# Optimization experiments

Hardware: AMD Instinct MI355X
Metric: run time of the kernel (lower is better)

## Reference

```python
import jax, jax.numpy as jnp
import numpy as np

FACTOR = 5      # ProbAttention sampling factor
NHEAD = 8
LN_EPS = 1e-5


def pos_encoding(L, d):
    pos = np.arange(L, dtype=np.float32)[:, None]
    div = np.exp(np.arange(0, d, 2, dtype=np.float32) * (-np.log(10000.0) / d))
    pe = np.zeros((L, d), np.float32)
    pe[:, 0::2] = np.sin(pos * div)
    pe[:, 1::2] = np.cos(pos * div)
    return jnp.asarray(pe)


def layer_norm(x, s, b):
    mu = x.mean(-1, keepdims=True)
    var = ((x - mu) ** 2).mean(-1, keepdims=True)
    return (x - mu) * jax.lax.rsqrt(var + LN_EPS) * s + b


def prob_attention(x4, key):
    # x4: [B, L, H, D]; self-attention (Q=K=V=x4), mask_flag=False
    B, L, H, D = x4.shape
    q = jnp.transpose(x4, (0, 2, 1, 3))  # [B,H,L,D]
    u = max(1, min(FACTOR * int(np.ceil(np.log(L))), L))  # L_Q == L_K
    # random K-sampling: per-query random subset of keys (shared across B,H)
    idx = jax.random.randint(key, (L, u), 0, L)
    k_s = q[:, :, idx, :]                                # [B,H,L,u,D] irregular gather
    qk_s = jnp.einsum('bhld,bhlsd->bhls', q, k_s)        # [B,H,L,u]
    M = qk_s.max(-1) - qk_s.sum(-1) / L                  # sparsity measure
    _, top = jax.lax.top_k(M, u)                         # [B,H,u] active queries
    q_red = jnp.take_along_axis(q, top[..., None], axis=2)   # [B,H,u,D]
    scale = 1.0 / jnp.sqrt(jnp.float32(D))
    scores = jnp.einsum('bhud,bhkd->bhuk', q_red, q) * scale  # reduced-query scores
    attn = jax.nn.softmax(scores, axis=-1)
    ctx_top = jnp.einsum('bhuk,bhkd->bhud', attn, q)     # V == q here
    # initial context = mean of V (mask_flag=False), scatter top-query results
    ctx = jnp.broadcast_to(q.mean(axis=2, keepdims=True), (B, H, L, D))
    bi = jnp.arange(B)[:, None, None]
    hi = jnp.arange(H)[None, :, None]
    ctx = ctx.at[bi, hi, top].set(ctx_top)
    return jnp.transpose(ctx, (0, 2, 1, 3))  # [B,L,H,D]


def encoder_layer(x4, ln1_s, ln1_b, w1, b1, w2, b2, ln2_s, ln2_b, key):
    B, L, H, D = x4.shape
    new = prob_attention(x4, key)
    x = x4.reshape(B, L, H * D)
    x = layer_norm(x + new.reshape(B, L, H * D), ln1_s, ln1_b)
    # conv1/conv2 with kernel_size=1 == pointwise linears
    y = jax.nn.gelu(jnp.einsum('bld,fd->blf', x, w1) + b1, approximate=False)
    y = jnp.einsum('blf,df->bld', y, w2) + b2
    x = layer_norm(x + y, ln2_s, ln2_b)
    return x.reshape(B, L, H, D)


def distil(x4, factor=2):
    # DistilledAttention: mean-pool over `factor` timesteps (zero-pad to multiple)
    B, L, H, D = x4.shape
    pad = (-L) % factor
    if pad:
        x4 = jnp.pad(x4, ((0, 0), (0, pad), (0, 0), (0, 0)))
    return x4.reshape(B, -1, factor, H, D).mean(axis=2)


def setup_inputs() -> dict:
    key = jax.random.key(0)
    B, L, IN, D, DF, NL = 8, 4096, 64, 512, 2048, 3
    ks = jax.random.split(key, 16)
    s = 0.02
    return {
        'x': jax.random.normal(ks[0], (B, L, IN), jnp.float32),
        'emb_w': jax.random.normal(ks[1], (D, IN), jnp.float32) * s,
        'emb_b': jnp.zeros((D,), jnp.float32),
        'ln1_s': jnp.ones((NL, D), jnp.float32),
        'ln1_b': jnp.zeros((NL, D), jnp.float32),
        'w1': jax.random.normal(ks[2], (NL, DF, D), jnp.float32) * s,
        'b1': jnp.zeros((NL, DF), jnp.float32),
        'w2': jax.random.normal(ks[3], (NL, D, DF), jnp.float32) * s,
        'b2': jnp.zeros((NL, D), jnp.float32),
        'ln2_s': jnp.ones((NL, D), jnp.float32),
        'ln2_b': jnp.zeros((NL, D), jnp.float32),
        'out_w': jax.random.normal(ks[4], (D, D), jnp.float32) * s,
        'out_b': jnp.zeros((D,), jnp.float32),
    }


def reference(x, emb_w, emb_b, ln1_s, ln1_b, w1, b1, w2, b2, ln2_s, ln2_b, out_w, out_b):
    B, L, _ = x.shape
    D = emb_w.shape[0]
    hd = D // NHEAD
    h = jnp.einsum('bli,di->bld', x, emb_w) + emb_b
    h = h + pos_encoding(L, D)[None]
    h = h.reshape(B, L, NHEAD, hd)
    NL = ln1_s.shape[0]
    rkey = jax.random.key(42)  # deterministic ProbSparse sampling
    for i in range(NL):
        h = encoder_layer(h, ln1_s[i], ln1_b[i], w1[i], b1[i], w2[i], b2[i],
                          ln2_s[i], ln2_b[i], jax.random.fold_in(rkey, i))
        if i < NL - 1:
            h = distil(h)
    B2, L2 = h.shape[:2]
    h = h.reshape(B2, L2, D)
    return jnp.einsum('bld,od->blo', h, out_w) + out_b
```

## Files before the change

kernel.cpp:

```cpp
#include <hip/hip_runtime.h>
#include <hip/hip_bf16.h>
#include <math.h>


typedef short short8 __attribute__((ext_vector_type(8)));
typedef float f32x4 __attribute__((ext_vector_type(4)));
typedef unsigned int uint;

__host__ __device__ inline void tf2x32(unsigned k0, unsigned k1,
                                       unsigned x0, unsigned x1,
                                       unsigned& o0, unsigned& o1) {
  unsigned ks2 = k0 ^ k1 ^ 0x1BD11BDAu;
#define TF_R(x, r) x0 += x1; x1 = ((x1 << (r)) | (x1 >> (32 - (r)))); x1 ^= x0;
  x0 += k0; x1 += k1;
  TF_R(x1,13) TF_R(x1,15) TF_R(x1,26) TF_R(x1,6)
  x0 += k1; x1 += ks2 + 1u;
  TF_R(x1,17) TF_R(x1,29) TF_R(x1,16) TF_R(x1,24)
  x0 += ks2; x1 += k0 + 2u;
  TF_R(x1,13) TF_R(x1,15) TF_R(x1,26) TF_R(x1,6)
  x0 += k0; x1 += k1 + 3u;
  TF_R(x1,17) TF_R(x1,29) TF_R(x1,16) TF_R(x1,24)
  x0 += k1; x1 += ks2 + 4u;
  TF_R(x1,13) TF_R(x1,15) TF_R(x1,26) TF_R(x1,6)
  x0 += ks2; x1 += k0 + 5u;
#undef TF_R
  o0 = x0; o1 = x1;
}

__global__ void k_idx(int* __restrict__ idx, unsigned k2a, unsigned k2b,
                      int n, int mask) {
  int j = blockIdx.x * 256 + threadIdx.x;
  if (j >= n) return;
  unsigned o0, o1;
  tf2x32(k2a, k2b, 0u, (unsigned)j, o0, o1);
  idx[j] = (int)((o0 ^ o1) & (unsigned)mask);
}

__global__ void k_pe(float* __restrict__ pe) {
  int t = blockIdx.x * 256 + threadIdx.x;
  int l = t >> 9, d = t & 511;
  double div = exp((double)(d & ~1) * (-9.210340371976184 / 512.0));
  double ang = (double)l * div;
  pe[t] = (float)((d & 1) ? cos(ang) : sin(ang));
}

__global__ __launch_bounds__(256) void k_embed(const float* __restrict__ x,
    const float* __restrict__ W, const float* __restrict__ eb,
    const float* __restrict__ pe, float* __restrict__ out) {
  __shared__ __align__(16) float xs[16][64];
  int r0 = blockIdx.x * 16;
  int t = threadIdx.x;
  ((float4*)&xs[0][0])[t] = ((const float4*)(x + (size_t)r0 * 64))[t];
  __syncthreads();
  int d0 = t, d1 = t + 256;
  float acc0[16], acc1[16];
#pragma unroll
  for (int r = 0; r < 16; r++) { acc0[r] = 0.f; acc1[r] = 0.f; }
  for (int k = 0; k < 64; k++) {
    float w0 = W[d0 * 64 + k], w1 = W[d1 * 64 + k];
#pragma unroll
    for (int r = 0; r < 16; r++) {
      float xv = xs[r][k];
      acc0[r] = fmaf(xv, w0, acc0[r]);
      acc1[r] = fmaf(xv, w1, acc1[r]);
    }
  }
  float eb0 = eb[d0], eb1 = eb[d1];
#pragma unroll
  for (int r = 0; r < 16; r++) {
    int row = r0 + r;
    int l = row & 4095;
    out[(size_t)row * 512 + d0] = acc0[r] + eb0 + pe[(size_t)l * 512 + d0];
    out[(size_t)row * 512 + d1] = acc1[r] + eb1 + pe[(size_t)l * 512 + d1];
  }
}

__global__ __launch_bounds__(256) void k_colmean1(const float* __restrict__ X,
    double* __restrict__ part, int L, int S) {
  int seg = blockIdx.x, bh = blockIdx.y, b = bh >> 3, h = bh & 7;
  int w = threadIdx.x >> 6, d = threadIdx.x & 63;
  int rows = L / S, r0 = seg * rows;
  const float* base = X + (size_t)b * L * 512 + h * 64 + d;
  double s = 0.0;
  for (int l = r0 + w; l < r0 + rows; l += 4) s += (double)base[(size_t)l * 512];
  __shared__ double red[4][64];
  red[w][d] = s;
  __syncthreads();
  if (w == 0)
    part[((size_t)bh * S + seg) * 64 + d] =
        red[0][d] + red[1][d] + red[2][d] + red[3][d];
}

__global__ void k_colmean2(const double* __restrict__ part,
    float* __restrict__ meanq, int L, int S) {
  int bh = blockIdx.x, d = threadIdx.x;
  const double* p = part + (size_t)bh * S * 64 + d;
  double s = 0.0;
  for (int seg = 0; seg < S; seg++) s += p[seg * 64];
  meanq[bh * 64 + d] = (float)(s / (double)L);
}

__global__ __launch_bounds__(256) void k_M(const float* __restrict__ X,
    const int* __restrict__ idx, float* __restrict__ Mout, int L, int Lsh,
    int u, float invL) {
  int w = threadIdx.x >> 6, lane = threadIdx.x & 63;
  int gl = blockIdx.x * 4 + w;
  int l = gl & (L - 1), bh = gl >> Lsh, b = bh >> 3, h = bh & 7;
  const float* Xbh = X + (size_t)b * L * 512 + h * 64;
  __shared__ float qs[4][64];
  qs[w][lane] = Xbh[(size_t)l * 512 + lane];
  __syncthreads();
  const int s16 = lane >> 2, j = lane & 3;
  float4 qv[4];
#pragma unroll
  for (int c = 0; c < 4; c++) qv[c] = *(const float4*)&qs[w][c * 16 + j * 4];
  const int base = l * u;
  int kx[3];
#pragma unroll
  for (int g = 0; g < 3; g++) {
    int s = g * 16 + s16;
    kx[g] = (s < u) ? idx[base + s] : 0;
  }
  float4 kv[3][4];
#pragma unroll
  for (int g = 0; g < 3; g++) {
    const float* row = Xbh + (size_t)kx[g] * 512 + j * 4;
#pragma unroll
    for (int c = 0; c < 4; c++) kv[g][c] = *(const float4*)(row + c * 16);
  }
  float mv = -1e30f, sv = 0.f;
#pragma unroll
  for (int g = 0; g < 3; g++) {
    float pc[4];
#pragma unroll
    for (int c = 0; c < 4; c++) {
      float p = qv[c].x * kv[g][c].x;
      p = fmaf(qv[c].y, kv[g][c].y, p);
      p = fmaf(qv[c].z, kv[g][c].z, p);
      p = fmaf(qv[c].w, kv[g][c].w, p);
      pc[c] = p;
    }
    float d = (pc[0] + pc[1]) + (pc[2] + pc[3]);
    d += __shfl_xor(d, 1);
    d += __shfl_xor(d, 2);
    if (g * 16 + s16 < u) { mv = fmaxf(mv, d); sv += d; }
  }
  for (int off = 4; off < 64; off <<= 1) {
    mv = fmaxf(mv, __shfl_xor(mv, off));
    sv += __shfl_xor(sv, off);
  }
  if (lane == 0) Mout[(size_t)bh * L + l] = mv - sv * invL;
}

__global__ __launch_bounds__(256) void k_topk(const float* __restrict__ M,
    int* __restrict__ top, int L, int u) {
  __shared__ float mv[4096];
  __shared__ float wv[4];
  __shared__ int wi[4];
  __shared__ int bi_s;
  int bh = blockIdx.x, t = threadIdx.x;
  int w = t >> 6, lane = t & 63;
  const float* Mr = M + (size_t)bh * L;
  for (int k = t; k < L; k += 256) mv[k] = Mr[k];
  __syncthreads();
  float lv = -1e30f; int li = 0x7fffffff;
  for (int k = t; k < L; k += 256) {
    float v = mv[k];
    if (v > lv) { lv = v; li = k; }
  }
  for (int it = 0; it < u; it++) {
    float v = lv; int i = li;
#pragma unroll
    for (int off = 1; off < 64; off <<= 1) {
      float v2 = __shfl_xor(v, off); int i2 = __shfl_xor(i, off);
      if (v2 > v || (v2 == v && i2 < i)) { v = v2; i = i2; }
    }
    if (lane == 0) { wv[w] = v; wi[w] = i; }
    __syncthreads();
    if (t == 0) {
      float bv = wv[0]; int bi = wi[0];
#pragma unroll
      for (int jj = 1; jj < 4; jj++) {
        if (wv[jj] > bv || (wv[jj] == bv && wi[jj] < bi)) { bv = wv[jj]; bi = wi[jj]; }
      }
      top[bh * u + it] = bi;
      mv[bi] = -1e30f;
      bi_s = bi;
    }
    __syncthreads();
    int bi = bi_s;
    if ((bi & 255) == t) {
      lv = -1e30f; li = 0x7fffffff;
      for (int k = t; k < L; k += 256) {
        float v = mv[k];
        if (v > lv) { lv = v; li = k; }
      }
    }
  }
}

__global__ void k_fill(float* __restrict__ A, const float* __restrict__ meanq, int L) {
  size_t t = (size_t)blockIdx.x * 256 + threadIdx.x;
  size_t e = t * 4;
  int dm = (int)(e & 511);
  int b = (int)((e >> 9) / (size_t)L);
  *(float4*)(A + e) = *(const float4*)(meanq + b * 512 + dm);
}

__global__ __launch_bounds__(256) void k_scores(const float* __restrict__ X,
    const int* __restrict__ top, float* __restrict__ S, int L, int u) {
  __shared__ __align__(16) float ktT[64][68];
  __shared__ __align__(16) float qred[48][64];
  int bh = blockIdx.y, b = bh >> 3, h = bh & 7;
  int k0 = blockIdx.x * 64;
  int t = threadIdx.x;
  const float* Xbh = X + (size_t)b * L * 512 + h * 64;
#pragma unroll
  for (int it = 0; it < 4; it++) {
    int lin = t + it * 256;
    int kk = lin >> 4, fi = lin & 15;
    float4 v = *(const float4*)(Xbh + (size_t)(k0 + kk) * 512 + fi * 4);
    ktT[fi * 4 + 0][kk] = v.x; ktT[fi * 4 + 1][kk] = v.y;
    ktT[fi * 4 + 2][kk] = v.z; ktT[fi * 4 + 3][kk] = v.w;
  }
#pragma unroll
  for (int it = 0; it < 3; it++) {
    int lin = t + it * 256;
    int ur = lin >> 4, fi = lin & 15;
    if (ur < u) {
      int row = top[bh * u + ur];
      *(float4*)(&qred[ur][fi * 4]) = *(const float4*)(Xbh + (size_t)row * 512 + fi * 4);
    } else if (ur < 48) {
      *(float4*)(&qred[ur][fi * 4]) = make_float4(0.f, 0.f, 0.f, 0.f);
    }
  }
  __syncthreads();
  int xq = t & 15, y = t >> 4;
  float acc[3][4];
#pragma unroll
  for (int j = 0; j < 3; j++)
#pragma unroll
    for (int e = 0; e < 4; e++) acc[j][e] = 0.f;
  for (int d = 0; d < 64; d++) {
    float4 kv = *(const float4*)(&ktT[d][xq * 4]);
#pragma unroll
    for (int j = 0; j < 3; j++) {
      float qv = qred[y * 3 + j][d];
      acc[j][0] = fmaf(qv, kv.x, acc[j][0]);
      acc[j][1] = fmaf(qv, kv.y, acc[j][1]);
      acc[j][2] = fmaf(qv, kv.z, acc[j][2]);
      acc[j][3] = fmaf(qv, kv.w, acc[j][3]);
    }
  }
#pragma unroll
  for (int j = 0; j < 3; j++) {
    int ur = y * 3 + j;
    if (ur < u) {
      float4 o = make_float4(acc[j][0] * 0.125f, acc[j][1] * 0.125f,
                             acc[j][2] * 0.125f, acc[j][3] * 0.125f);
      *(float4*)(S + ((size_t)(bh * u + ur)) * L + k0 + xq * 4) = o;
    }
  }
}

__global__ __launch_bounds__(256) void k_smstat(const float* __restrict__ S,
    float* __restrict__ MX, double* __restrict__ INV, int L, int u) {
  int ur = blockIdx.x, bh = blockIdx.y;
  const float* Srow = S + ((size_t)(bh * u + ur)) * L;
  int t = threadIdx.x;
  __shared__ float rm[256];
  __shared__ double rs[256];
  float m = -1e30f;
  for (int k = t; k < L; k += 256) m = fmaxf(m, Srow[k]);
  rm[t] = m; __syncthreads();
  for (int off = 128; off; off >>= 1) {
    if (t < off) rm[t] = fmaxf(rm[t], rm[t + off]);
    __syncthreads();
  }
  float mx = rm[0];
  double s = 0.0;
  for (int k = t; k < L; k += 256) s += (double)expf(Srow[k] - mx);
  rs[t] = s; __syncthreads();
  for (int off = 128; off; off >>= 1) {
    if (t < off) rs[t] += rs[t + off];
    __syncthreads();
  }
  if (t == 0) { MX[bh * 48 + ur] = mx; INV[bh * 48 + ur] = 1.0 / rs[0]; }
}

#define PVSEG 8
__global__ __launch_bounds__(256) void k_pv(const float* __restrict__ X,
    const float* __restrict__ S, const float* __restrict__ MX,
    float* __restrict__ P2, int L, int u) {
  __shared__ __align__(16) float xs[32][64];
  __shared__ __align__(16) float wsm[32][52];
  int seg = blockIdx.x, bh = blockIdx.y, b = bh >> 3, h = bh & 7;
  int t = threadIdx.x, w = t >> 6, lane = t & 63;
  int rows = L / PVSEG, l0 = seg * rows;
  const float* Xb = X + (size_t)b * L * 512 + h * 64;
  int li = lane & 31, par = lane >> 5;
  const float* Sp[6]; float mxl[6]; int val[6];
#pragma unroll
  for (int jj = 0; jj < 6; jj++) {
    int ur = w * 12 + par + jj * 2;
    val[jj] = (ur < u);
    Sp[jj] = S + (size_t)(bh * u + (val[jj] ? ur : 0)) * L + l0 + li;
    mxl[jj] = val[jj] ? MX[bh * 48 + ur] : 0.f;
  }
  float acc[12];
#pragma unroll
  for (int j = 0; j < 12; j++) acc[j] = 0.f;
  int xr = t >> 4, xf = t & 15;
  for (int c = 0; c < rows; c += 32) {
    __syncthreads();
    *(float4*)&xs[xr][xf * 4] =
        *(const float4*)(Xb + (size_t)(l0 + c + xr) * 512 + xf * 4);
    *(float4*)&xs[16 + xr][xf * 4] =
        *(const float4*)(Xb + (size_t)(l0 + c + 16 + xr) * 512 + xf * 4);
#pragma unroll
    for (int jj = 0; jj < 6; jj++) {
      float e = val[jj] ? expf(Sp[jj][c] - mxl[jj]) : 0.f;
      wsm[li][w * 12 + par + jj * 2] = e;
    }
    __syncthreads();
#pragma unroll 2
    for (int l = 0; l < 32; l++) {
      float xv = xs[l][lane];
      float4 w0 = *(const float4*)&wsm[l][w * 12];
      float4 w1 = *(const float4*)&wsm[l][w * 12 + 4];
      float4 w2 = *(const float4*)&wsm[l][w * 12 + 8];
      acc[0]  = fmaf(w0.x, xv, acc[0]);  acc[1]  = fmaf(w0.y, xv, acc[1]);
      acc[2]  = fmaf(w0.z, xv, acc[2]);  acc[3]  = fmaf(w0.w, xv, acc[3]);
      acc[4]  = fmaf(w1.x, xv, acc[4]);  acc[5]  = fmaf(w1.y, xv, acc[5]);
      acc[6]  = fmaf(w1.z, xv, acc[6]);  acc[7]  = fmaf(w1.w, xv, acc[7]);
      acc[8]  = fmaf(w2.x, xv, acc[8]);  acc[9]  = fmaf(w2.y, xv, acc[9]);
      acc[10] = fmaf(w2.z, xv, acc[10]); acc[11] = fmaf(w2.w, xv, acc[11]);
    }
  }
  float* P = P2 + ((size_t)(bh * PVSEG + seg) * 48 + w * 12) * 64 + lane;
#pragma unroll
  for (int j = 0; j < 12; j++) P[j * 64] = acc[j];
}

__global__ __launch_bounds__(256) void k_pvred(const float* __restrict__ P2,
    const double* __restrict__ INV, const int* __restrict__ top,
    float* __restrict__ A, int L, int u) {
  int bh = blockIdx.x, b = bh >> 3, h = bh & 7;
  const float* Pb = P2 + (size_t)bh * PVSEG * 48 * 64;
  for (int e = threadIdx.x; e < u * 64; e += 256) {
    int ur = e >> 6, d = e & 63;
    const float* p = Pb + ur * 64 + d;
    const int st = 48 * 64;
    double s = ((double)p[0] + (double)p[st]) +
               ((double)p[2 * st] + (double)p[3 * st]) +
               ((double)p[4 * st] + (double)p[5 * st]) +
               ((double)p[6 * st] + (double)p[7 * st]);
    double tot = s * INV[bh * 48 + ur];
    int row = top[bh * u + ur];
    A[((size_t)b * L + row) * 512 + h * 64 + d] = (float)tot;
  }
}

__global__ __launch_bounds__(256) void k_ln1(float* __restrict__ X,
    const float* __restrict__ A, const float* __restrict__ gs,
    const float* __restrict__ gb) {
  int w = threadIdx.x >> 6, lane = threadIdx.x & 63;
  int row = blockIdx.x * 4 + w;
  float* xr = X + (size_t)row * 512;
  const float* ar = A + (size_t)row * 512;
  float v[8]; double s = 0.0, s2 = 0.0;
#pragma unroll
  for (int i = 0; i < 8; i++) {
    float val = xr[lane + i * 64] + ar[lane + i * 64];
    v[i] = val; s += (double)val; s2 += (double)val * (double)val;
  }
  for (int off = 32; off; off >>= 1) { s += __shfl_xor(s, off); s2 += __shfl_xor(s2, off); }
  double mu = s * (1.0 / 512.0);
  double var = s2 * (1.0 / 512.0) - mu * mu;
  float rsd = (float)(1.0 / sqrt(var + 1e-5));
  float muf = (float)mu;
#pragma unroll
  for (int i = 0; i < 8; i++) {
    int d = lane + i * 64;
    xr[d] = (v[i] - muf) * rsd * gs[d] + gb[d];
  }
}

__global__ __launch_bounds__(256) void k_ln2(const float* __restrict__ X,
    const float* __restrict__ Y2, const float* __restrict__ gs,
    const float* __restrict__ gb, float* __restrict__ out, int pool) {
  int w = threadIdx.x >> 6, lane = threadIdx.x & 63;
  int orow = blockIdx.x * 4 + w;
  float o[8] = {0.f,0.f,0.f,0.f,0.f,0.f,0.f,0.f};
  int reps = pool ? 2 : 1;
  for (int p = 0; p < reps; p++) {
    int row = pool ? (orow * 2 + p) : orow;
    const float* xr = X + (size_t)row * 512;
    const float* yr = Y2 + (size_t)row * 512;
    float v[8]; double s = 0.0, s2 = 0.0;
#pragma unroll
    for (int i = 0; i < 8; i++) {
      float val = xr[lane + i * 64] + yr[lane + i * 64];
      v[i] = val; s += (double)val; s2 += (double)val * (double)val;
    }
    for (int off = 32; off; off >>= 1) { s += __shfl_xor(s, off); s2 += __shfl_xor(s2, off); }
    double mu = s * (1.0 / 512.0);
    double var = s2 * (1.0 / 512.0) - mu * mu;
    float rsd = (float)(1.0 / sqrt(var + 1e-5));
    float muf = (float)mu;
#pragma unroll
    for (int i = 0; i < 8; i++)
      o[i] += (v[i] - muf) * rsd * gs[lane + i * 64] + gb[lane + i * 64];
  }
  float sc = pool ? 0.5f : 1.0f;
#pragma unroll
  for (int i = 0; i < 8; i++)
    out[(size_t)orow * 512 + lane + i * 64] = o[i] * sc;
}


__device__ inline unsigned bsplit(float x, float y, float& rx, float& ry) {
  union { __hip_bfloat162 h; unsigned u; } c;
  c.h = __float22bfloat162_rn(make_float2(x, y));
  rx = x - __uint_as_float(c.u << 16);
  ry = y - __uint_as_float(c.u & 0xffff0000u);
  return c.u;
}

__device__ inline void split2u(float4 v0, float4 v1, uint4& H, uint4& M) {
  float r[8]; float d0, d1;
  H.x = bsplit(v0.x, v0.y, r[0], r[1]);
  H.y = bsplit(v0.z, v0.w, r[2], r[3]);
  H.z = bsplit(v1.x, v1.y, r[4], r[5]);
  H.w = bsplit(v1.z, v1.w, r[6], r[7]);
  M.x = bsplit(r[0], r[1], d0, d1);
  M.y = bsplit(r[2], r[3], d0, d1);
  M.z = bsplit(r[4], r[5], d0, d1);
  M.w = bsplit(r[6], r[7], d0, d1);
}

__global__ void k_splitX(const float* __restrict__ X, char* __restrict__ P,
                         int K, int total8) {
  int f = blockIdx.x * 256 + threadIdx.x;
  if (f >= total8) return;
  int k8 = f % (K >> 3), m = f / (K >> 3);
  int k = k8 * 8;
  const float* src = X + (size_t)m * K + k;
  float4 v0 = *(const float4*)(src);
  float4 v1 = *(const float4*)(src + 4);
  uint4 H, Md;
  split2u(v0, v1, H, Md);
  size_t psz = (size_t)total8 * 16;
  size_t off = ((size_t)(m >> 4) * (K >> 5) + (k >> 5)) * 1024
             + (size_t)(((k >> 3) & 3) * 256 + (m & 15) * 16);
  *(uint4*)(P + off) = H;
  *(uint4*)(P + psz + off) = Md;
}

__device__ __forceinline__ void async16(void* lds, const void* g) {
  __builtin_amdgcn_global_load_lds(
      (const __attribute__((address_space(1))) uint*)g,
      (__attribute__((address_space(3))) uint*)lds, 16, 0, 0);
}

template <int MT, int GELU, int PLANES_OUT, int CMODE>
__global__ __launch_bounds__(256) void k_gemm6(const char* __restrict__ AP,
    const char* __restrict__ BP, const float* __restrict__ bias,
    void* __restrict__ Cout, int N, int K, int kt0, int kt1) {
  __shared__ __align__(16) char lds[(MT * 2 + 16) * 1024];
  const int t = threadIdx.x;
  const int w = t >> 6, lane = t & 63;
  const int bx = blockIdx.x, by = blockIdx.y;
  const int quad = lane >> 4, rit = lane & 15;
  const int Mrows = gridDim.y * (MT * 16);
  const size_t psA = (size_t)Mrows * K * 2;
  const size_t psB = (size_t)N * K * 2;
  const int KB = K >> 5;
  char* ldsA = lds;
  char* ldsB = lds + MT * 2 * 1024;
  const int wm = (w >> 1) * (MT / 2), wn = (w & 1) * 4;
  f32x4 acc[MT / 2][4];
#pragma unroll
  for (int i = 0; i < MT / 2; i++)
#pragma unroll
    for (int j = 0; j < 4; j++) acc[i][j] = (f32x4){0.f, 0.f, 0.f, 0.f};
  for (int kt = kt0; kt < kt1; kt++) {
#pragma unroll
    for (int r = 0; r < MT / 2; r++) {
      int q = w + 4 * r;
      int p = q / MT, tt = q % MT;
      async16(ldsA + (p * MT + tt) * 1024,
              AP + p * psA + ((size_t)(by * MT + tt) * KB + kt) * 1024 + lane * 16);
    }
#pragma unroll
    for (int r = 0; r < 4; r++) {
      int q = w + 4 * r;
      int p = q >> 3, tt = q & 7;
      async16(ldsB + (p * 8 + tt) * 1024,
              BP + p * psB + ((size_t)(bx * 8 + tt) * KB + kt) * 1024 + lane * 16);
    }
    __syncthreads();
    short8 af[2][MT / 2];
#pragma unroll
    for (int p = 0; p < 2; p++)
#pragma unroll
      for (int mi = 0; mi < MT / 2; mi++)
        af[p][mi] = *(const short8*)(ldsA + (p * MT + wm + mi) * 1024 + lane * 16);
#pragma unroll
    for (int ni = 0; ni < 4; ni++) {
      const char* bb = ldsB + (wn + ni) * 1024 + lane * 16;
      short8 bh = *(const short8*)(bb);
      short8 bm = *(const short8*)(bb + 8192);
#pragma unroll
      for (int mi = 0; mi < MT / 2; mi++) {
        f32x4 c = acc[mi][ni];
        c = __builtin_amdgcn_mfma_f32_16x16x32_bf16(af[0][mi], bh, c, 0, 0, 0);
        c = __builtin_amdgcn_mfma_f32_16x16x32_bf16(af[0][mi], bm, c, 0, 0, 0);
        c = __builtin_amdgcn_mfma_f32_16x16x32_bf16(af[1][mi], bh, c, 0, 0, 0);
        acc[mi][ni] = c;
      }
    }
    __syncthreads();
  }
  const int n0 = bx * 128, m_base = by * (MT * 16);
  if (CMODE == 1) {
    float* C = (float*)Cout;
#pragma unroll
    for (int mi = 0; mi < MT / 2; mi++) {
      const int gr0 = m_base + (wm + mi) * 16 + quad * 4;
#pragma unroll
      for (int ni = 0; ni < 4; ni++) {
        const int gc = n0 + (wn + ni) * 16 + rit;
#pragma unroll
        for (int e = 0; e < 4; e++)
          C[(size_t)(gr0 + e) * N + gc] = acc[mi][ni][e];
      }
    }
  } else if (CMODE == 2) {
    float* C = (float*)Cout;
#pragma unroll
    for (int mi = 0; mi < MT / 2; mi++) {
      const int gr0 = m_base + (wm + mi) * 16 + quad * 4;
#pragma unroll
      for (int ni = 0; ni < 4; ni++) {
        const int gc = n0 + (wn + ni) * 16 + rit;
        const float bia = bias[gc];
#pragma unroll
        for (int e = 0; e < 4; e++) {
          size_t ix = (size_t)(gr0 + e) * N + gc;
          C[ix] = (C[ix] + acc[mi][ni][e]) + bia;
        }
      }
    }
  } else if (!PLANES_OUT) {
    float* C = (float*)Cout;
#pragma unroll
    for (int mi = 0; mi < MT / 2; mi++) {
      const int gr0 = m_base + (wm + mi) * 16 + quad * 4;
#pragma unroll
      for (int ni = 0; ni < 4; ni++) {
        const int gc = n0 + (wn + ni) * 16 + rit;
        const float bia = bias[gc];
#pragma unroll
        for (int e = 0; e < 4; e++) {
          float v = acc[mi][ni][e] + bia;
          if (GELU) v = 0.5f * v * (1.0f + erff(v * 0.7071067811865476f));
          C[(size_t)(gr0 + e) * N + gc] = v;
        }
      }
    }
  } else {
    char* CP = (char*)Cout;
    const size_t psC = (size_t)Mrows * N * 2;
    float* lf = (float*)lds;
    for (int h = 0; h < 2; h++) {
      __syncthreads();
      if ((w & 1) == h) {
#pragma unroll
        for (int ni = 0; ni < 4; ni++) {
          const float bia = bias[n0 + h * 64 + ni * 16 + rit];
#pragma unroll
          for (int mi = 0; mi < MT / 2; mi++) {
            const int ml0 = (wm + mi) * 16 + quad * 4;
#pragma unroll
            for (int e = 0; e < 4; e++) {
              float v = acc[mi][ni][e] + bia;
              if (GELU) v = 0.5f * v * (1.0f + erff(v * 0.7071067811865476f));
              lf[(ml0 + e) * 64 + ni * 16 + rit] = v;
            }
          }
        }
      }
      __syncthreads();
#pragma unroll
      for (int it = 0; it < (MT * 16 * 8) / 256; it++) {
        int p = it * 256 + t;
        int ml = p >> 3, n8 = p & 7;
        float4 v0 = *(const float4*)&lf[ml * 64 + n8 * 8];
        float4 v1 = *(const float4*)&lf[ml * 64 + n8 * 8 + 4];
        uint4 H, Md;
        split2u(v0, v1, H, Md);
        int mg = m_base + ml, kg = n0 + h * 64 + n8 * 8;
        size_t off = ((size_t)(mg >> 4) * (N >> 5) + (kg >> 5)) * 1024
                   + (size_t)(((kg >> 3) & 3) * 256 + (mg & 15) * 16);
        *(uint4*)(CP + off) = H;
        *(uint4*)(CP + psC + off) = Md;
      }
    }
  }
}

extern "C" void kernel_launch(void* const* d_in, const int* in_sizes, int n_in,
                              void* d_out, int out_size, void* d_ws, size_t ws_size,
                              hipStream_t stream) {
  const float* x     = (const float*)d_in[0];
  const float* emb_w = (const float*)d_in[1];
  const float* emb_b = (const float*)d_in[2];
  const float* ln1_s = (const float*)d_in[3];
  const float* ln1_b = (const float*)d_in[4];
  const float* w1    = (const float*)d_in[5];
  const float* b1    = (const float*)d_in[6];
  const float* w2    = (const float*)d_in[7];
  const float* b2    = (const float*)d_in[8];
  const float* ln2_s = (const float*)d_in[9];
  const float* ln2_b = (const float*)d_in[10];
  const float* out_w = (const float*)d_in[11];
  const float* out_b = (const float*)d_in[12];
  float* outp = (float*)d_out;

  char* ws = (char*)d_ws;
  if (ws_size < (212ULL << 20)) return;
  float* PE    = (float*)(ws);
  char*  W1S   = ws;
  float* BUF[3] = { (float*)(ws + (8ULL << 20)),
                    (float*)(ws + (72ULL << 20)),
                    (float*)(ws + (136ULL << 20)) };
  char*  W2S   = ws + (200ULL << 20);
  float* MB    = (float*)(ws + (206ULL << 20));
  int*   IDX   = (int*)  (ws + (207ULL << 20));
  int*   TOP   = (int*)  (ws + (208ULL << 20));
  float* MEANQ = (float*)(ws + (208ULL << 20) + (64 << 10));
  float* MXB   = (float*)(ws + (208ULL << 20) + (128 << 10));
  double* INVB = (double*)(ws + (208ULL << 20) + (192 << 10));
  double* PART = (double*)(ws + (209ULL << 20));

  k_pe<<<4096 * 512 / 256, 256, 0, stream>>>(PE);
  k_embed<<<(8 * 4096) / 16, 256, 0, stream>>>(x, emb_w, emb_b, PE, BUF[0]);

  const int Ls[3] = {4096, 2048, 1024};
  const int Lshs[3] = {12, 11, 10};
  const int us[3] = {45, 40, 35};
  int xi = 0, ai = 1, yi = 2;
  for (int layer = 0; layer < 3; layer++) {
    const int L = Ls[layer], u = us[layer];
    float* X = BUF[xi]; float* A = BUF[ai]; float* Y = BUF[yi];

    k_splitX<<<(2048 * 512 / 8) / 256, 256, 0, stream>>>(
        w1 + (size_t)layer * 2048 * 512, W1S, 512, 2048 * 512 / 8);
    k_splitX<<<(512 * 2048 / 8) / 256, 256, 0, stream>>>(
        w2 + (size_t)layer * 512 * 2048, W2S, 2048, 512 * 2048 / 8);

    unsigned Ka, Kb, k2a, k2b;
    tf2x32(0u, 42u, 0u, (unsigned)layer, Ka, Kb);
    tf2x32(Ka, Kb, 0u, 1u, k2a, k2b);
    const int n = L * u;
    k_idx<<<(n + 255) / 256, 256, 0, stream>>>(IDX, k2a, k2b, n, L - 1);
    const int S = 32;
    k_colmean1<<<dim3(S, 64), 256, 0, stream>>>(X, PART, L, S);
    k_colmean2<<<64, 64, 0, stream>>>(PART, MEANQ, L, S);
    k_M<<<64 * L / 4, 256, 0, stream>>>(X, IDX, MB, L, Lshs[layer], u,
                                        1.0f / (float)L);
    k_topk<<<64, 256, 0, stream>>>(MB, TOP, L, u);
    k_fill<<<8 * L / 2, 256, 0, stream>>>(A, MEANQ, L);
    k_scores<<<dim3(L / 64, 64), 256, 0, stream>>>(X, TOP, Y, L, u);
    float* P2 = (float*)((char*)Y + (48ULL << 20));
    k_smstat<<<dim3(u, 64), 256, 0, stream>>>(Y, MXB, INVB, L, u);
    k_pv<<<dim3(PVSEG, 64), 256, 0, stream>>>(X, Y, MXB, P2, L, u);
    k_pvred<<<64, 256, 0, stream>>>(P2, INVB, TOP, A, L, u);
    k_ln1<<<8 * L / 4, 256, 0, stream>>>(X, A, ln1_s + layer * 512, ln1_b + layer * 512);

    char* YP = (char*)Y;
    const int chunks = (8 * L) / 8192;
    for (int c = 0; c < chunks; c++) {
      const float* Xc = X + (size_t)c * 8192 * 512;
      float* Ac = A + (size_t)c * 8192 * 512;
      char* XP = (char*)Ac;
      k_splitX<<<(8192 * 512 / 8) / 256, 256, 0, stream>>>(
          Xc, XP, 512, 8192 * 512 / 8);
      k_gemm6<8, 1, 1, 0><<<dim3(16, 64), 256, 0, stream>>>(
          XP, W1S, b1 + layer * 2048, YP, 2048, 512, 0, 16);
      k_gemm6<4, 0, 0, 1><<<dim3(4, 128), 256, 0, stream>>>(
          YP, W2S, b2 + layer * 512, Ac, 512, 2048, 0, 32);
      k_gemm6<4, 0, 0, 2><<<dim3(4, 128), 256, 0, stream>>>(
          YP, W2S, b2 + layer * 512, Ac, 512, 2048, 32, 64);
    }
    if (layer < 2)
      k_ln2<<<8 * (L / 2) / 4, 256, 0, stream>>>(X, A, ln2_s + layer * 512,
                                                 ln2_b + layer * 512, Y, 1);
    else
      k_ln2<<<8 * L / 4, 256, 0, stream>>>(X, A, ln2_s + layer * 512,
                                           ln2_b + layer * 512, Y, 0);
    int tswap = xi; xi = yi; yi = ai; ai = tswap;
  }
  char* XFP = (char*)BUF[ai];
  char* WOS = W2S;
  k_splitX<<<(512 * 512 / 8) / 256, 256, 0, stream>>>(out_w, WOS, 512, 512 * 512 / 8);
  k_splitX<<<(8192 * 512 / 8) / 256, 256, 0, stream>>>(BUF[xi], XFP, 512, 8192 * 512 / 8);
  k_gemm6<4, 0, 0, 1><<<dim3(4, 128), 256, 0, stream>>>(
      XFP, WOS, out_b, outp, 512, 512, 0, 8);
  k_gemm6<4, 0, 0, 2><<<dim3(4, 128), 256, 0, stream>>>(
      XFP, WOS, out_b, outp, 512, 512, 8, 16);
}
```

Before: 2.328 ms.

## Replace dense mean-fill with per-row flags and merge split-K GEMM launches

The full-size k_fill of the attention context buffer is removed. k_pvred now records which (bh,row) entries hold top-query results in a byte flag array, and k_ln1 picks either the scattered result or the per-batch mean on the fly. Separately, the second GEMM and the output GEMM were each run as two launches splitting K in halves, with a read-modify-write epilogue on the second; they now run as one full-K launch that writes once. This removes a large buffer write and an extra pass over C, but it adds a memset plus byte loads per element in LN1, and it drops the K split that may have served precision or occupancy.

```diff
diff --git a/kernel.cpp b/kernel.cpp
--- a/kernel.cpp
+++ b/kernel.cpp
@@ -199,14 +199,6 @@
   }
 }
 
-__global__ void k_fill(float* __restrict__ A, const float* __restrict__ meanq, int L) {
-  size_t t = (size_t)blockIdx.x * 256 + threadIdx.x;
-  size_t e = t * 4;
-  int dm = (int)(e & 511);
-  int b = (int)((e >> 9) / (size_t)L);
-  *(float4*)(A + e) = *(const float4*)(meanq + b * 512 + dm);
-}
-
 __global__ __launch_bounds__(256) void k_scores(const float* __restrict__ X,
     const int* __restrict__ top, float* __restrict__ S, int L, int u) {
   __shared__ __align__(16) float ktT[64][68];
@@ -344,7 +336,7 @@
 
 __global__ __launch_bounds__(256) void k_pvred(const float* __restrict__ P2,
     const double* __restrict__ INV, const int* __restrict__ top,
-    float* __restrict__ A, int L, int u) {
+    float* __restrict__ A, char* __restrict__ FLG, int L, int u) {
   int bh = blockIdx.x, b = bh >> 3, h = bh & 7;
   const float* Pb = P2 + (size_t)bh * PVSEG * 48 * 64;
   for (int e = threadIdx.x; e < u * 64; e += 256) {
@@ -358,20 +350,27 @@
     double tot = s * INV[bh * 48 + ur];
     int row = top[bh * u + ur];
     A[((size_t)b * L + row) * 512 + h * 64 + d] = (float)tot;
+    if (d == 0) FLG[(size_t)bh * L + row] = 1;
   }
 }
 
 __global__ __launch_bounds__(256) void k_ln1(float* __restrict__ X,
-    const float* __restrict__ A, const float* __restrict__ gs,
-    const float* __restrict__ gb) {
+    const float* __restrict__ A, const char* __restrict__ FLG,
+    const float* __restrict__ meanq, const float* __restrict__ gs,
+    const float* __restrict__ gb, int L, int Lsh) {
   int w = threadIdx.x >> 6, lane = threadIdx.x & 63;
   int row = blockIdx.x * 4 + w;
+  int b = row >> Lsh, l = row & (L - 1);
   float* xr = X + (size_t)row * 512;
   const float* ar = A + (size_t)row * 512;
+  const float* mq = meanq + b * 512;
+  const char* fg = FLG + ((size_t)b * 8) * L + l;
   float v[8]; double s = 0.0, s2 = 0.0;
 #pragma unroll
   for (int i = 0; i < 8; i++) {
-    float val = xr[lane + i * 64] + ar[lane + i * 64];
+    int d = lane + i * 64;
+    float ctx = fg[(size_t)i * L] ? ar[d] : mq[d];
+    float val = xr[d] + ctx;
     v[i] = val; s += (double)val; s2 += (double)val * (double)val;
   }
   for (int off = 32; off; off >>= 1) { s += __shfl_xor(s, off); s2 += __shfl_xor(s2, off); }
@@ -463,10 +462,10 @@
       (__attribute__((address_space(3))) uint*)lds, 16, 0, 0);
 }
 
-template <int MT, int GELU, int PLANES_OUT, int CMODE>
+template <int MT, int GELU, int PLANES_OUT>
 __global__ __launch_bounds__(256) void k_gemm6(const char* __restrict__ AP,
     const char* __restrict__ BP, const float* __restrict__ bias,
-    void* __restrict__ Cout, int N, int K, int kt0, int kt1) {
+    void* __restrict__ Cout, int N, int K) {
   __shared__ __align__(16) char lds[(MT * 2 + 16) * 1024];
   const int t = threadIdx.x;
   const int w = t >> 6, lane = t & 63;
@@ -484,7 +483,7 @@
   for (int i = 0; i < MT / 2; i++)
 #pragma unroll
     for (int j = 0; j < 4; j++) acc[i][j] = (f32x4){0.f, 0.f, 0.f, 0.f};
-  for (int kt = kt0; kt < kt1; kt++) {
+  for (int kt = 0; kt < KB; kt++) {
 #pragma unroll
     for (int r = 0; r < MT / 2; r++) {
       int q = w + 4 * r;
@@ -523,36 +522,7 @@
     __syncthreads();
   }
   const int n0 = bx * 128, m_base = by * (MT * 16);
-  if (CMODE == 1) {
-    float* C = (float*)Cout;
-#pragma unroll
-    for (int mi = 0; mi < MT / 2; mi++) {
-      const int gr0 = m_base + (wm + mi) * 16 + quad * 4;
-#pragma unroll
-      for (int ni = 0; ni < 4; ni++) {
-        const int gc = n0 + (wn + ni) * 16 + rit;
-#pragma unroll
-        for (int e = 0; e < 4; e++)
-          C[(size_t)(gr0 + e) * N + gc] = acc[mi][ni][e];
-      }
-    }
-  } else if (CMODE == 2) {
-    float* C = (float*)Cout;
-#pragma unroll
-    for (int mi = 0; mi < MT / 2; mi++) {
-      const int gr0 = m_base + (wm + mi) * 16 + quad * 4;
-#pragma unroll
-      for (int ni = 0; ni < 4; ni++) {
-        const int gc = n0 + (wn + ni) * 16 + rit;
-        const float bia = bias[gc];
-#pragma unroll
-        for (int e = 0; e < 4; e++) {
-          size_t ix = (size_t)(gr0 + e) * N + gc;
-          C[ix] = (C[ix] + acc[mi][ni][e]) + bia;
-        }
-      }
-    }
-  } else if (!PLANES_OUT) {
+  if (!PLANES_OUT) {
     float* C = (float*)Cout;
 #pragma unroll
     for (int mi = 0; mi < MT / 2; mi++) {
@@ -643,6 +613,7 @@
   float* MXB   = (float*)(ws + (208ULL << 20) + (128 << 10));
   double* INVB = (double*)(ws + (208ULL << 20) + (192 << 10));
   double* PART = (double*)(ws + (209ULL << 20));
+  char*  FLG   = ws + (210ULL << 20);
 
   k_pe<<<4096 * 512 / 256, 256, 0, stream>>>(PE);
   k_embed<<<(8 * 4096) / 16, 256, 0, stream>>>(x, emb_w, emb_b, PE, BUF[0]);
@@ -671,13 +642,15 @@
     k_M<<<64 * L / 4, 256, 0, stream>>>(X, IDX, MB, L, Lshs[layer], u,
                                         1.0f / (float)L);
     k_topk<<<64, 256, 0, stream>>>(MB, TOP, L, u);
-    k_fill<<<8 * L / 2, 256, 0, stream>>>(A, MEANQ, L);
+    hipMemsetAsync(FLG, 0, (size_t)64 * L, stream);
     k_scores<<<dim3(L / 64, 64), 256, 0, stream>>>(X, TOP, Y, L, u);
     float* P2 = (float*)((char*)Y + (48ULL << 20));
     k_smstat<<<dim3(u, 64), 256, 0, stream>>>(Y, MXB, INVB, L, u);
     k_pv<<<dim3(PVSEG, 64), 256, 0, stream>>>(X, Y, MXB, P2, L, u);
-    k_pvred<<<64, 256, 0, stream>>>(P2, INVB, TOP, A, L, u);
-    k_ln1<<<8 * L / 4, 256, 0, stream>>>(X, A, ln1_s + layer * 512, ln1_b + layer * 512);
+    k_pvred<<<64, 256, 0, stream>>>(P2, INVB, TOP, A, FLG, L, u);
+    k_ln1<<<8 * L / 4, 256, 0, stream>>>(X, A, FLG, MEANQ,
+                                         ln1_s + layer * 512,
+                                         ln1_b + layer * 512, L, Lshs[layer]);
 
     char* YP = (char*)Y;
     const int chunks = (8 * L) / 8192;
@@ -687,12 +660,10 @@
       char* XP = (char*)Ac;
       k_splitX<<<(8192 * 512 / 8) / 256, 256, 0, stream>>>(
           Xc, XP, 512, 8192 * 512 / 8);
-      k_gemm6<8, 1, 1, 0><<<dim3(16, 64), 256, 0, stream>>>(
-          XP, W1S, b1 + layer * 2048, YP, 2048, 512, 0, 16);
-      k_gemm6<4, 0, 0, 1><<<dim3(4, 128), 256, 0, stream>>>(
-          YP, W2S, b2 + layer * 512, Ac, 512, 2048, 0, 32);
-      k_gemm6<4, 0, 0, 2><<<dim3(4, 128), 256, 0, stream>>>(
-          YP, W2S, b2 + layer * 512, Ac, 512, 2048, 32, 64);
+      k_gemm6<8, 1, 1><<<dim3(16, 64), 256, 0, stream>>>(
+          XP, W1S, b1 + layer * 2048, YP, 2048, 512);
+      k_gemm6<4, 0, 0><<<dim3(4, 128), 256, 0, stream>>>(
+          YP, W2S, b2 + layer * 512, Ac, 512, 2048);
     }
     if (layer < 2)
       k_ln2<<<8 * (L / 2) / 4, 256, 0, stream>>>(X, A, ln2_s + layer * 512,
@@ -706,8 +677,6 @@
   char* WOS = W2S;
   k_splitX<<<(512 * 512 / 8) / 256, 256, 0, stream>>>(out_w, WOS, 512, 512 * 512 / 8);
   k_splitX<<<(8192 * 512 / 8) / 256, 256, 0, stream>>>(BUF[xi], XFP, 512, 8192 * 512 / 8);
-  k_gemm6<4, 0, 0, 1><<<dim3(4, 128), 256, 0, stream>>>(
-      XFP, WOS, out_b, outp, 512, 512, 0, 8);
-  k_gemm6<4, 0, 0, 2><<<dim3(4, 128), 256, 0, stream>>>(
-      XFP, WOS, out_b, outp, 512, 512, 8, 16);
-}
+  k_gemm6<4, 0, 0><<<dim3(4, 128), 256, 0, stream>>>(
+      XFP, WOS, out_b, outp, 512, 512);
+}
```

After: 2.215 ms. 4.9% less time.
